# Optimization experiments

Hardware: AMD Instinct MI355X
Metric: run time of the kernel (lower is better)

Reference implementation:

```python
import jax, jax.numpy as jnp
import numpy as np

N = 50000
E = 800000
IN_CH = 128
HID = 64
HEADS = 4
OUT_CH = 64
NEG_SLOPE = 0.2


def add_self_loops(edge_index, num_nodes):
    loops = jnp.arange(num_nodes, dtype=edge_index.dtype)
    src = jnp.concatenate([edge_index[0], loops])
    dst = jnp.concatenate([edge_index[1], loops])
    return src, dst


def gat_layer(x, src, dst, W, a_src, a_dst, b, heads, out_ch, concat):
    n = x.shape[0]
    h = (x @ W).reshape(n, heads, out_ch)              # [N,H,C]
    al_src = jnp.einsum('nhc,hc->nh', h, a_src)        # [N,H]
    al_dst = jnp.einsum('nhc,hc->nh', h, a_dst)        # [N,H]
    e = jax.nn.leaky_relu(al_src[src] + al_dst[dst], NEG_SLOPE)  # [Et,H]
    # segment softmax over incoming edges of each destination node
    m = jax.ops.segment_max(e, dst, num_segments=n)
    ex = jnp.exp(e - m[dst])
    denom = jax.ops.segment_sum(ex, dst, num_segments=n)
    alpha = ex / (denom[dst] + 1e-16)                  # [Et,H]
    msg = h[src] * alpha[:, :, None]                   # [Et,H,C]
    out = jax.ops.segment_sum(msg, dst, num_segments=n)  # [N,H,C]
    if concat:
        out = out.reshape(n, heads * out_ch)
    else:
        out = out.mean(axis=1)
    return out + b


def setup_inputs() -> dict:
    key = jax.random.key(0)
    ks = jax.random.split(key, 10)
    x = jax.random.normal(ks[0], (N, IN_CH), dtype=jnp.float32)
    edge_index = jax.random.randint(ks[1], (2, E), 0, N, dtype=jnp.int64)
    s1 = 1.0 / np.sqrt(IN_CH)
    W1 = jax.random.normal(ks[2], (IN_CH, HEADS * HID), dtype=jnp.float32) * s1
    a_src1 = jax.random.normal(ks[3], (HEADS, HID), dtype=jnp.float32) * 0.1
    a_dst1 = jax.random.normal(ks[4], (HEADS, HID), dtype=jnp.float32) * 0.1
    b1 = jnp.zeros((HEADS * HID,), dtype=jnp.float32)
    s2 = 1.0 / np.sqrt(HEADS * HID)
    W2 = jax.random.normal(ks[5], (HEADS * HID, OUT_CH), dtype=jnp.float32) * s2
    a_src2 = jax.random.normal(ks[6], (1, OUT_CH), dtype=jnp.float32) * 0.1
    a_dst2 = jax.random.normal(ks[7], (1, OUT_CH), dtype=jnp.float32) * 0.1
    b2 = jnp.zeros((OUT_CH,), dtype=jnp.float32)
    return {"x": x, "edge_index": edge_index, "W1": W1, "a_src1": a_src1,
            "a_dst1": a_dst1, "b1": b1, "W2": W2, "a_src2": a_src2,
            "a_dst2": a_dst2, "b2": b2}


def reference(x, edge_index, W1, a_src1, a_dst1, b1, W2, a_src2, a_dst2, b2):
    src, dst = add_self_loops(edge_index, x.shape[0])
    h = gat_layer(x, src, dst, W1, a_src1, a_dst1, b1, HEADS, HID, True)
    h = jax.nn.elu(h)
    h = gat_layer(h, src, dst, W2, a_src2, a_dst2, b2, 1, OUT_CH, False)
    return jax.nn.elu(h)
```

## Files before the change

### kernel.cpp

```cpp
#include <hip/hip_runtime.h>
#include <hip/hip_bf16.h>
#include <cstdint>
#include <cstddef>


typedef float f32x4 __attribute__((ext_vector_type(4)));
typedef __fp16 f16x8 __attribute__((ext_vector_type(8)));
typedef __fp16 f16x4 __attribute__((ext_vector_type(4)));

static __device__ __forceinline__ float lrelu02(float x) { return x > 0.f ? x : 0.2f * x; }
static __device__ __forceinline__ float eluf(float x)    { return x > 0.f ? x : __expf(x) - 1.f; }

__global__ void detect_kernel(const int* __restrict__ ei, int* __restrict__ flag, int e) {
    int lane = threadIdx.x;
    int m = e < 64 ? e : 64;
    int z = (lane < m && ei[2 * lane + 1] == 0) ? 1 : 0;
    unsigned long long bal = __ballot(z);
    if (lane == 0) *flag = (__popcll(bal) >= m / 2 + 1) ? 1 : 0;
}

__global__ void hist_kernel(const int* __restrict__ ei, const int* __restrict__ flag,
                            int* __restrict__ deg, int e) {
    int i = blockIdx.x * 256 + threadIdx.x;
    if (i < e) {
        int f = *flag;
        int d = f ? ei[2 * (e + i)] : ei[e + i];
        atomicAdd(&deg[d], 1);
    }
}

__global__ __launch_bounds__(256) void scan_blocks_kernel(const int* __restrict__ deg,
                                                          int* __restrict__ loc,
                                                          int* __restrict__ bsum, int n) {
    __shared__ int wsum[4];
    int t = threadIdx.x, lane = t & 63, w = t >> 6;
    int base = blockIdx.x * 1024 + t * 4;
    int4 v = make_int4(0, 0, 0, 0);
    if (base + 3 < n) {
        v = *(const int4*)(deg + base);
        v.x += 1; v.y += 1; v.z += 1; v.w += 1;
    } else {
        if (base < n) v.x = deg[base] + 1;
        if (base + 1 < n) v.y = deg[base + 1] + 1;
        if (base + 2 < n) v.z = deg[base + 2] + 1;
        if (base + 3 < n) v.w = deg[base + 3] + 1;
    }
    int s = v.x + v.y + v.z + v.w;
    int incl = s;
    #pragma unroll
    for (int d = 1; d < 64; d <<= 1) { int o = __shfl_up(incl, d); if (lane >= d) incl += o; }
    if (lane == 63) wsum[w] = incl;
    __syncthreads();
    int woff = 0;
    for (int k = 0; k < w; ++k) woff += wsum[k];
    int excl = woff + incl - s;
    if (base < n) {
        int e0 = excl, e1 = e0 + v.x, e2 = e1 + v.y, e3 = e2 + v.z;
        loc[base] = e0;
        if (base + 1 < n) loc[base + 1] = e1;
        if (base + 2 < n) loc[base + 2] = e2;
        if (base + 3 < n) loc[base + 3] = e3;
    }
    if (t == 255) bsum[blockIdx.x] = woff + incl;
}

__global__ __launch_bounds__(256) void scan_sums_kernel(const int* __restrict__ bsum,
                                                        int* __restrict__ boff, int nb,
                                                        int* __restrict__ rowptr, int n) {
    __shared__ int ws[4];
    int t = threadIdx.x, lane = t & 63, w = t >> 6;
    int v = (t < nb) ? bsum[t] : 0;
    int incl = v;
    #pragma unroll
    for (int d = 1; d < 64; d <<= 1) { int o = __shfl_up(incl, d); if (lane >= d) incl += o; }
    if (lane == 63) ws[w] = incl;
    __syncthreads();
    int woff = 0;
    for (int k = 0; k < w; ++k) woff += ws[k];
    int excl = woff + incl - v;
    if (t < nb) boff[t] = excl;
    if (t == nb - 1) rowptr[n] = excl + v;
}

__global__ void scan_add_kernel(int* __restrict__ rowptr, const int* __restrict__ boff,
                                int* __restrict__ cursor, int n) {
    int i = blockIdx.x * 256 + threadIdx.x;
    if (i < n) {
        int v = rowptr[i] + boff[i >> 10];
        rowptr[i] = v;
        cursor[i] = v;
    }
}

__global__ void scatter_kernel(const int* __restrict__ ei, const int* __restrict__ flag,
                               int* __restrict__ cursor, int* __restrict__ sidx,
                               int e, int et) {
    int i = blockIdx.x * 256 + threadIdx.x;
    if (i >= et) return;
    int s, d;
    if (i < e) {
        int f = *flag;
        s = f ? ei[2 * i] : ei[i];
        d = f ? ei[2 * (e + i)] : ei[e + i];
    } else { s = d = i - e; }
    int pos = atomicAdd(&cursor[d], 1);
    sidx[pos] = s;
}

__global__ void prep_kernel(const float* __restrict__ W1, const float* __restrict__ W2,
                            __fp16* __restrict__ w1t, __fp16* __restrict__ w2t) {
    int i = blockIdx.x * 256 + threadIdx.x;
    if (i < 32768) {
        int nn = i >> 7, k = i & 127;
        w1t[i] = (__fp16)W1[k * 256 + nn];
    } else {
        int j = i - 32768;
        int nn = j >> 8, k = j & 255;
        w2t[j] = (__fp16)W2[k * 64 + nn];
    }
}

__global__ __launch_bounds__(256) void gemm1_kernel(const float* __restrict__ A,
                                                    const __fp16* __restrict__ w1t,
                                                    __fp16* __restrict__ C,
                                                    const float* __restrict__ a_src,
                                                    const float* __restrict__ a_dst,
                                                    float* __restrict__ als,
                                                    float* __restrict__ ald, int M) {
    __shared__ __fp16 sm[24064];
    #define AS(r, c)  sm[(r) * 72 + (c)]
    #define BST(r, c) sm[4608 + (r) * 72 + (c)]
    #define CS(r, c)  sm[(r) * 264 + (c)]
    float* sa = (float*)(sm + 23040);
    float* sd = (float*)(sm + 23552);
    int t = threadIdx.x;
    int wv = t >> 6, l = t & 63;
    int lm = l & 15, kq = l >> 4;
    int bm = blockIdx.x * 64;
    sa[t] = a_src[t];
    sd[t] = a_dst[t];
    f32x4 zero = {0.f, 0.f, 0.f, 0.f};
    f32x4 acc[4][4] = {{zero, zero, zero, zero}, {zero, zero, zero, zero},
                       {zero, zero, zero, zero}, {zero, zero, zero, zero}};
    int arow = t >> 2, akp = (t & 3) * 16;
    for (int k0 = 0; k0 < 128; k0 += 64) {
        {
            int gr = bm + arow;
            f16x8 av0, av1;
            if (gr < M) {
                const float* ap = A + (size_t)gr * 128 + k0 + akp;
                float4 a0 = *(const float4*)(ap + 0);
                float4 a1 = *(const float4*)(ap + 4);
                float4 a2 = *(const float4*)(ap + 8);
                float4 a3 = *(const float4*)(ap + 12);
                av0[0] = (__fp16)a0.x; av0[1] = (__fp16)a0.y; av0[2] = (__fp16)a0.z; av0[3] = (__fp16)a0.w;
                av0[4] = (__fp16)a1.x; av0[5] = (__fp16)a1.y; av0[6] = (__fp16)a1.z; av0[7] = (__fp16)a1.w;
                av1[0] = (__fp16)a2.x; av1[1] = (__fp16)a2.y; av1[2] = (__fp16)a2.z; av1[3] = (__fp16)a2.w;
                av1[4] = (__fp16)a3.x; av1[5] = (__fp16)a3.y; av1[6] = (__fp16)a3.z; av1[7] = (__fp16)a3.w;
            } else {
                f16x8 z = {0,0,0,0,0,0,0,0}; av0 = z; av1 = z;
            }
            *(f16x8*)&AS(arow, akp) = av0;
            *(f16x8*)&AS(arow, akp + 8) = av1;
        }
        {
            const __fp16* bp = w1t + (size_t)t * 128 + k0;
            #pragma unroll
            for (int c = 0; c < 8; ++c)
                *(f16x8*)&BST(t, c * 8) = *(const f16x8*)(bp + c * 8);
        }
        __syncthreads();
        #pragma unroll
        for (int ki = 0; ki < 2; ++ki) {
            int kc = ki * 32 + kq * 8;
            f16x8 af[4];
            #pragma unroll
            for (int mt = 0; mt < 4; ++mt) af[mt] = *(const f16x8*)&AS(mt * 16 + lm, kc);
            #pragma unroll
            for (int nt = 0; nt < 4; ++nt) {
                f16x8 bfrag = *(const f16x8*)&BST(wv * 64 + nt * 16 + lm, kc);
                #pragma unroll
                for (int mt = 0; mt < 4; ++mt)
                    acc[mt][nt] = __builtin_amdgcn_mfma_f32_16x16x32_f16(af[mt], bfrag, acc[mt][nt], 0, 0, 0);
            }
        }
        __syncthreads();
    }
    #pragma unroll
    for (int mt = 0; mt < 4; ++mt)
        #pragma unroll
        for (int nt = 0; nt < 4; ++nt)
            #pragma unroll
            for (int r = 0; r < 4; ++r)
                CS(mt * 16 + kq * 4 + r, wv * 64 + nt * 16 + lm) = (__fp16)acc[mt][nt][r];
    __syncthreads();
    {
        int row = t >> 2, head = t & 3;
        int gr = bm + row;
        f16x8 c[8];
        #pragma unroll
        for (int q = 0; q < 8; ++q) c[q] = *(const f16x8*)&CS(row, head * 64 + q * 8);
        float ps = 0.f, pd = 0.f;
        #pragma unroll
        for (int q = 0; q < 8; ++q)
            #pragma unroll
            for (int j = 0; j < 8; ++j) {
                float v = (float)c[q][j];
                ps += v * sa[head * 64 + q * 8 + j];
                pd += v * sd[head * 64 + q * 8 + j];
            }
        if (gr < M) {
            f16x8* gp = (f16x8*)(C + (size_t)gr * 256 + head * 64);
            #pragma unroll
            for (int q = 0; q < 8; ++q) gp[q] = c[q];
            als[gr * 4 + head] = ps;
            ald[gr * 4 + head] = pd;
        }
    }
    #undef AS
    #undef BST
    #undef CS
}

__global__ __launch_bounds__(256) void gemm2_kernel(const __fp16* __restrict__ A,
                                                    const __fp16* __restrict__ w2t,
                                                    __fp16* __restrict__ C,
                                                    const float* __restrict__ a_src,
                                                    const float* __restrict__ a_dst,
                                                    float* __restrict__ als,
                                                    float* __restrict__ ald, int M) {
    __shared__ __fp16 sm[9216];
    #define AS(r, c)  sm[(r) * 72 + (c)]
    #define BST(r, c) sm[4608 + (r) * 72 + (c)]
    #define CS(r, c)  sm[(r) * 72 + (c)]
    int t = threadIdx.x;
    int wv = t >> 6, l = t & 63;
    int lm = l & 15, kq = l >> 4;
    int bm = blockIdx.x * 64;
    f32x4 zero = {0.f, 0.f, 0.f, 0.f};
    f32x4 acc[4] = {zero, zero, zero, zero};
    int arow = t >> 2, akp = (t & 3) * 16;
    int bn = t & 63, bkc = (t >> 6) * 16;
    for (int k0 = 0; k0 < 256; k0 += 64) {
        {
            int gr = bm + arow;
            f16x8 av0, av1;
            if (gr < M) {
                const __fp16* ap = A + (size_t)gr * 256 + k0 + akp;
                av0 = *(const f16x8*)(ap);
                av1 = *(const f16x8*)(ap + 8);
            } else { f16x8 z = {0,0,0,0,0,0,0,0}; av0 = z; av1 = z; }
            *(f16x8*)&AS(arow, akp) = av0;
            *(f16x8*)&AS(arow, akp + 8) = av1;
        }
        {
            const __fp16* bp = w2t + (size_t)bn * 256 + k0 + bkc;
            *(f16x8*)&BST(bn, bkc) = *(const f16x8*)(bp);
            *(f16x8*)&BST(bn, bkc + 8) = *(const f16x8*)(bp + 8);
        }
        __syncthreads();
        #pragma unroll
        for (int ki = 0; ki < 2; ++ki) {
            int kc = ki * 32 + kq * 8;
            f16x8 bfrag = *(const f16x8*)&BST(wv * 16 + lm, kc);
            #pragma unroll
            for (int mt = 0; mt < 4; ++mt) {
                f16x8 afrag = *(const f16x8*)&AS(mt * 16 + lm, kc);
                acc[mt] = __builtin_amdgcn_mfma_f32_16x16x32_f16(afrag, bfrag, acc[mt], 0, 0, 0);
            }
        }
        __syncthreads();
    }
    #pragma unroll
    for (int mt = 0; mt < 4; ++mt)
        #pragma unroll
        for (int r = 0; r < 4; ++r)
            CS(mt * 16 + kq * 4 + r, wv * 16 + lm) = (__fp16)acc[mt][r];
    __syncthreads();
    {
        int row = t >> 2, ch = (t & 3) * 16;
        int gr = bm + row;
        f16x8 c0 = *(const f16x8*)&CS(row, ch);
        f16x8 c1 = *(const f16x8*)&CS(row, ch + 8);
        if (gr < M) {
            f16x8* gp = (f16x8*)(C + (size_t)gr * 64 + ch);
            gp[0] = c0; gp[1] = c1;
        }
        float ps = 0.f, pd = 0.f;
        #pragma unroll
        for (int j = 0; j < 8; ++j) {
            float v0 = (float)c0[j], v1 = (float)c1[j];
            ps += v0 * a_src[ch + j] + v1 * a_src[ch + 8 + j];
            pd += v0 * a_dst[ch + j] + v1 * a_dst[ch + 8 + j];
        }
        ps += __shfl_down(ps, 2); ps += __shfl_down(ps, 1);
        pd += __shfl_down(pd, 2); pd += __shfl_down(pd, 1);
        if ((t & 3) == 0 && gr < M) {
            als[gr] = ps;
            ald[gr] = pd;
        }
    }
    #undef AS
    #undef BST
    #undef CS
}

__global__ __launch_bounds__(256) void agg1_kernel(const __fp16* __restrict__ h1,
                                                   const int* __restrict__ sidx,
                                                   const int* __restrict__ rowptr,
                                                   const float* __restrict__ als,
                                                   const float* __restrict__ ald,
                                                   const float* __restrict__ b1,
                                                   __fp16* __restrict__ x2, int n) {
    int t = threadIdx.x, wv = t >> 6, l = t & 63;
    int node = blockIdx.x * 4 + wv;
    if (node >= n) return;
    int le = l & 31, halfE = l >> 5;
    int head = le >> 3;
    float aldn = ald[node * 4 + head];
    int p0 = rowptr[node], p1 = rowptr[node + 1];
    float acc[8] = {0.f, 0.f, 0.f, 0.f, 0.f, 0.f, 0.f, 0.f};
    float accw = 0.f;
    auto body = [&](int p) {
        int s = sidx[p];
        float wt = __expf(lrelu02(als[s * 4 + head] + aldn));
        accw += wt;
        f16x8 r = *(const f16x8*)(h1 + (size_t)s * 256 + le * 8);
        #pragma unroll
        for (int j = 0; j < 8; ++j) acc[j] += wt * (float)r[j];
    };
    int p = p0 + halfE;
    for (; p + 6 < p1; p += 8) { body(p); body(p + 2); body(p + 4); body(p + 6); }
    for (; p < p1; p += 2) body(p);
    #pragma unroll
    for (int j = 0; j < 8; ++j) acc[j] += __shfl_down(acc[j], 32);
    accw += __shfl_down(accw, 32);
    if (l < 32) {
        float rd = 1.f / (accw + 1e-16f);
        f16x8 o;
        #pragma unroll
        for (int j = 0; j < 8; ++j) {
            float v = acc[j] * rd + b1[le * 8 + j];
            o[j] = (__fp16)eluf(v);
        }
        *(f16x8*)(x2 + (size_t)node * 256 + le * 8) = o;
    }
}

__global__ __launch_bounds__(256) void agg2_kernel(const __fp16* __restrict__ h2,
                                                   const int* __restrict__ sidx,
                                                   const int* __restrict__ rowptr,
                                                   const float* __restrict__ als,
                                                   const float* __restrict__ ald,
                                                   const float* __restrict__ b2,
                                                   float* __restrict__ out, int n) {
    int t = threadIdx.x, wv = t >> 6, l = t & 63;
    int node = blockIdx.x * 4 + wv;
    if (node >= n) return;
    int slot = l >> 3, cq = l & 7;
    float aldn = ald[node];
    int p0 = rowptr[node], p1 = rowptr[node + 1];
    float acc[8] = {0.f, 0.f, 0.f, 0.f, 0.f, 0.f, 0.f, 0.f};
    float accw = 0.f;
    auto body = [&](int p) {
        int s = sidx[p];
        float wt = __expf(lrelu02(als[s] + aldn));
        accw += wt;
        f16x8 r = *(const f16x8*)(h2 + (size_t)s * 64 + cq * 8);
        #pragma unroll
        for (int j = 0; j < 8; ++j) acc[j] += wt * (float)r[j];
    };
    int p = p0 + slot;
    for (; p + 8 < p1; p += 16) { body(p); body(p + 8); }
    if (p < p1) body(p);
    #pragma unroll
    for (int j = 0; j < 8; ++j) {
        acc[j] += __shfl_down(acc[j], 32);
        acc[j] += __shfl_down(acc[j], 16);
        acc[j] += __shfl_down(acc[j], 8);
    }
    accw += __shfl_down(accw, 32);
    accw += __shfl_down(accw, 16);
    accw += __shfl_down(accw, 8);
    if (l < 8) {
        float rd = 1.f / (accw + 1e-16f);
        float4 o0, o1;
        o0.x = eluf(acc[0] * rd + b2[cq * 8 + 0]);
        o0.y = eluf(acc[1] * rd + b2[cq * 8 + 1]);
        o0.z = eluf(acc[2] * rd + b2[cq * 8 + 2]);
        o0.w = eluf(acc[3] * rd + b2[cq * 8 + 3]);
        o1.x = eluf(acc[4] * rd + b2[cq * 8 + 4]);
        o1.y = eluf(acc[5] * rd + b2[cq * 8 + 5]);
        o1.z = eluf(acc[6] * rd + b2[cq * 8 + 6]);
        o1.w = eluf(acc[7] * rd + b2[cq * 8 + 7]);
        float4* gp = (float4*)(out + (size_t)node * 64 + cq * 8);
        gp[0] = o0; gp[1] = o1;
    }
}

extern "C" void kernel_launch(void* const* d_in, const int* in_sizes, int n_in,
                              void* d_out, int out_size, void* d_ws, size_t ws_size,
                              hipStream_t stream) {
    const float* x   = (const float*)d_in[0];
    const int*   ei  = (const int*)d_in[1];
    const float* W1  = (const float*)d_in[2];
    const float* as1 = (const float*)d_in[3];
    const float* ad1 = (const float*)d_in[4];
    const float* b1  = (const float*)d_in[5];
    const float* W2  = (const float*)d_in[6];
    const float* as2 = (const float*)d_in[7];
    const float* ad2 = (const float*)d_in[8];
    const float* b2  = (const float*)d_in[9];
    float* out = (float*)d_out;

    const int n  = in_sizes[0] / 128;
    const int e  = in_sizes[1] / 2;
    const int et = e + n;

    char* w = (char*)d_ws;
    size_t off = 0;
    auto take = [&](size_t bytes) -> void* {
        void* p = w + off;
        off = (off + bytes + 255) & ~(size_t)255;
        return p;
    };
    __fp16* h1h = (__fp16*)take((size_t)n * 256 * 2);
    __fp16* x2h = (__fp16*)take((size_t)n * 256 * 2);
    __fp16* h2h = (__fp16*)take((size_t)n * 64 * 2);
    __fp16* w1t = (__fp16*)take((size_t)256 * 128 * 2);
    __fp16* w2t = (__fp16*)take((size_t)64 * 256 * 2);
    float* al1s = (float*)take((size_t)n * 4 * 4);
    float* al1d = (float*)take((size_t)n * 4 * 4);
    float* al2s = (float*)take((size_t)n * 4);
    float* al2d = (float*)take((size_t)n * 4);
    int* deg    = (int*)take((size_t)(n + 1) * 4);
    int* rowptr = (int*)take((size_t)(n + 1) * 4);
    int* cursor = (int*)take((size_t)(n + 1) * 4);
    int* sidx   = (int*)take((size_t)et * 4);
    int* bsum   = (int*)take(1024);
    int* boff   = (int*)take(1024);
    int* flag   = (int*)take(256);

    detect_kernel<<<1, 64, 0, stream>>>(ei, flag, e);
    hipMemsetAsync(deg, 0, (size_t)n * 4, stream);
    prep_kernel<<<192, 256, 0, stream>>>(W1, W2, w1t, w2t);
    hist_kernel<<<(e + 255) / 256, 256, 0, stream>>>(ei, flag, deg, e);
    int nb = (n + 1023) / 1024;
    scan_blocks_kernel<<<nb, 256, 0, stream>>>(deg, rowptr, bsum, n);
    scan_sums_kernel<<<1, 256, 0, stream>>>(bsum, boff, nb, rowptr, n);
    scan_add_kernel<<<(n + 255) / 256, 256, 0, stream>>>(rowptr, boff, cursor, n);
    scatter_kernel<<<(et + 255) / 256, 256, 0, stream>>>(ei, flag, cursor, sidx, e, et);

    const int mblocks = (n + 63) / 64;
    const int nodeblocks = (n + 3) / 4;

    gemm1_kernel<<<mblocks, 256, 0, stream>>>(x, w1t, h1h, as1, ad1, al1s, al1d, n);
    agg1_kernel<<<nodeblocks, 256, 0, stream>>>(h1h, sidx, rowptr, al1s, al1d, b1, x2h, n);

    gemm2_kernel<<<mblocks, 256, 0, stream>>>(x2h, w2t, h2h, as2, ad2, al2s, al2d, n);
    agg2_kernel<<<nodeblocks, 256, 0, stream>>>(h2h, sidx, rowptr, al2s, al2d, b2, out, n);
}
```

Measured before the change: 310.3 us.

## Fuse layer-1 aggregation with layer-2 GEMM and trim CSR-build launches

Layer-1 aggregation now writes each 32-node block's ELU output into shared memory, and the layer-2 projection runs there with MFMA. This removes the x2 intermediate's global write and read and one kernel launch. The edge-layout detect kernel, the deg memset and the block-sum scan kernel are folded into neighbouring kernels: each block recomputes the layout flag, and scan_add loops over the block sums. The agg2 loop is unrolled further. The fused kernel uses 512 threads with large shared memory, which may lower occupancy during the gather-heavy aggregation.

```diff
diff --git a/kernel.cpp b/kernel.cpp
--- a/kernel.cpp
+++ b/kernel.cpp
@@ -6,24 +6,45 @@
 
 typedef float f32x4 __attribute__((ext_vector_type(4)));
 typedef __fp16 f16x8 __attribute__((ext_vector_type(8)));
-typedef __fp16 f16x4 __attribute__((ext_vector_type(4)));
 
 static __device__ __forceinline__ float lrelu02(float x) { return x > 0.f ? x : 0.2f * x; }
 static __device__ __forceinline__ float eluf(float x)    { return x > 0.f ? x : __expf(x) - 1.f; }
 
-__global__ void detect_kernel(const int* __restrict__ ei, int* __restrict__ flag, int e) {
-    int lane = threadIdx.x;
-    int m = e < 64 ? e : 64;
-    int z = (lane < m && ei[2 * lane + 1] == 0) ? 1 : 0;
-    unsigned long long bal = __ballot(z);
-    if (lane == 0) *flag = (__popcll(bal) >= m / 2 + 1) ? 1 : 0;
-}
-
-__global__ void hist_kernel(const int* __restrict__ ei, const int* __restrict__ flag,
-                            int* __restrict__ deg, int e) {
+static __device__ __forceinline__ int block_flag(const int* __restrict__ ei, int e,
+                                                 int* sflag) {
+    int t = threadIdx.x;
+    if (t < 64) {
+        int m = e < 64 ? e : 64;
+        int z = (t < m && ei[2 * t + 1] == 0) ? 1 : 0;
+        unsigned long long bal = __ballot(z);
+        if (t == 0) *sflag = (__popcll(bal) >= m / 2 + 1) ? 1 : 0;
+    }
+    __syncthreads();
+    return *sflag;
+}
+
+__global__ void prep_kernel(const float* __restrict__ W1, const float* __restrict__ W2,
+                            __fp16* __restrict__ w1t, __fp16* __restrict__ w2t,
+                            int* __restrict__ deg, int n) {
+    int i = blockIdx.x * 256 + threadIdx.x;
+    if (i < 32768) {
+        int nn = i >> 7, k = i & 127;
+        w1t[i] = (__fp16)W1[k * 256 + nn];
+    } else if (i < 49152) {
+        int j = i - 32768;
+        int nn = j >> 8, k = j & 255;
+        w2t[j] = (__fp16)W2[k * 64 + nn];
+    } else if (i - 49152 <= n) {
+        deg[i - 49152] = 0;
+    }
+}
+
+__global__ __launch_bounds__(256) void hist_kernel(const int* __restrict__ ei,
+                                                   int* __restrict__ deg, int e) {
+    __shared__ int sflag;
+    int f = block_flag(ei, e, &sflag);
     int i = blockIdx.x * 256 + threadIdx.x;
     if (i < e) {
-        int f = *flag;
         int d = f ? ei[2 * (e + i)] : ei[e + i];
         atomicAdd(&deg[d], 1);
     }
@@ -64,60 +85,38 @@
     if (t == 255) bsum[blockIdx.x] = woff + incl;
 }
 
-__global__ __launch_bounds__(256) void scan_sums_kernel(const int* __restrict__ bsum,
-                                                        int* __restrict__ boff, int nb,
-                                                        int* __restrict__ rowptr, int n) {
-    __shared__ int ws[4];
-    int t = threadIdx.x, lane = t & 63, w = t >> 6;
-    int v = (t < nb) ? bsum[t] : 0;
-    int incl = v;
-    #pragma unroll
-    for (int d = 1; d < 64; d <<= 1) { int o = __shfl_up(incl, d); if (lane >= d) incl += o; }
-    if (lane == 63) ws[w] = incl;
-    __syncthreads();
-    int woff = 0;
-    for (int k = 0; k < w; ++k) woff += ws[k];
-    int excl = woff + incl - v;
-    if (t < nb) boff[t] = excl;
-    if (t == nb - 1) rowptr[n] = excl + v;
-}
-
-__global__ void scan_add_kernel(int* __restrict__ rowptr, const int* __restrict__ boff,
-                                int* __restrict__ cursor, int n) {
+__global__ void scan_add_kernel(int* __restrict__ rowptr, const int* __restrict__ bsum,
+                                int* __restrict__ cursor, int n, int nb) {
     int i = blockIdx.x * 256 + threadIdx.x;
     if (i < n) {
-        int v = rowptr[i] + boff[i >> 10];
+        int chunk = i >> 10;
+        int off = 0;
+        for (int k = 0; k < chunk; ++k) off += bsum[k];
+        int v = rowptr[i] + off;
         rowptr[i] = v;
         cursor[i] = v;
-    }
-}
-
-__global__ void scatter_kernel(const int* __restrict__ ei, const int* __restrict__ flag,
-                               int* __restrict__ cursor, int* __restrict__ sidx,
-                               int e, int et) {
+    } else if (i == n) {
+        int tot = 0;
+        for (int k = 0; k < nb; ++k) tot += bsum[k];
+        rowptr[n] = tot;
+    }
+}
+
+__global__ __launch_bounds__(256) void scatter_kernel(const int* __restrict__ ei,
+                                                      int* __restrict__ cursor,
+                                                      int* __restrict__ sidx,
+                                                      int e, int et) {
+    __shared__ int sflag;
+    int f = block_flag(ei, e, &sflag);
     int i = blockIdx.x * 256 + threadIdx.x;
     if (i >= et) return;
     int s, d;
     if (i < e) {
-        int f = *flag;
         s = f ? ei[2 * i] : ei[i];
         d = f ? ei[2 * (e + i)] : ei[e + i];
     } else { s = d = i - e; }
     int pos = atomicAdd(&cursor[d], 1);
     sidx[pos] = s;
-}
-
-__global__ void prep_kernel(const float* __restrict__ W1, const float* __restrict__ W2,
-                            __fp16* __restrict__ w1t, __fp16* __restrict__ w2t) {
-    int i = blockIdx.x * 256 + threadIdx.x;
-    if (i < 32768) {
-        int nn = i >> 7, k = i & 127;
-        w1t[i] = (__fp16)W1[k * 256 + nn];
-    } else {
-        int j = i - 32768;
-        int nn = j >> 8, k = j & 255;
-        w2t[j] = (__fp16)W2[k * 64 + nn];
-    }
 }
 
 __global__ __launch_bounds__(256) void gemm1_kernel(const float* __restrict__ A,
@@ -222,129 +221,106 @@
     #undef CS
 }
 
-__global__ __launch_bounds__(256) void gemm2_kernel(const __fp16* __restrict__ A,
-                                                    const __fp16* __restrict__ w2t,
-                                                    __fp16* __restrict__ C,
-                                                    const float* __restrict__ a_src,
-                                                    const float* __restrict__ a_dst,
-                                                    float* __restrict__ als,
-                                                    float* __restrict__ ald, int M) {
-    __shared__ __fp16 sm[9216];
-    #define AS(r, c)  sm[(r) * 72 + (c)]
-    #define BST(r, c) sm[4608 + (r) * 72 + (c)]
-    #define CS(r, c)  sm[(r) * 72 + (c)]
-    int t = threadIdx.x;
-    int wv = t >> 6, l = t & 63;
+__global__ __launch_bounds__(512) void agg1g2_kernel(const __fp16* __restrict__ h1,
+                                                     const int* __restrict__ sidx,
+                                                     const int* __restrict__ rowptr,
+                                                     const float* __restrict__ als,
+                                                     const float* __restrict__ ald,
+                                                     const float* __restrict__ b1,
+                                                     const __fp16* __restrict__ w2t,
+                                                     const float* __restrict__ a_src2,
+                                                     const float* __restrict__ a_dst2,
+                                                     __fp16* __restrict__ h2,
+                                                     float* __restrict__ al2s,
+                                                     float* __restrict__ al2d, int n) {
+    __shared__ __fp16 X[32 * 264];
+    __shared__ __fp16 Bs[64 * 264];
+    #define XS(r, c)  X[(r) * 264 + (c)]
+    #define BS2(r, c) Bs[(r) * 264 + (c)]
+    #define CS2(r, c) X[(r) * 72 + (c)]
+    int t = threadIdx.x, wv = t >> 6, l = t & 63;
+    int bm = blockIdx.x * 32;
+    {
+        int nn = t >> 3, kc = (t & 7) * 32;
+        const __fp16* bp = w2t + (size_t)nn * 256 + kc;
+        #pragma unroll
+        for (int c = 0; c < 4; ++c)
+            *(f16x8*)&BS2(nn, kc + c * 8) = *(const f16x8*)(bp + c * 8);
+    }
+    int le = l & 31, halfE = l >> 5, head = le >> 3;
+    #pragma unroll
+    for (int q = 0; q < 4; ++q) {
+        int row = wv * 4 + q;
+        int node = bm + row;
+        float acc[8] = {0.f, 0.f, 0.f, 0.f, 0.f, 0.f, 0.f, 0.f};
+        float accw = 0.f;
+        if (node < n) {
+            float aldn = ald[node * 4 + head];
+            int p0 = rowptr[node], p1 = rowptr[node + 1];
+            auto body = [&](int p) {
+                int s = sidx[p];
+                float wt = __expf(lrelu02(als[s * 4 + head] + aldn));
+                accw += wt;
+                f16x8 r = *(const f16x8*)(h1 + (size_t)s * 256 + le * 8);
+                #pragma unroll
+                for (int j = 0; j < 8; ++j) acc[j] += wt * (float)r[j];
+            };
+            int p = p0 + halfE;
+            for (; p + 6 < p1; p += 8) { body(p); body(p + 2); body(p + 4); body(p + 6); }
+            for (; p < p1; p += 2) body(p);
+        }
+        #pragma unroll
+        for (int j = 0; j < 8; ++j) acc[j] += __shfl_down(acc[j], 32);
+        accw += __shfl_down(accw, 32);
+        if (l < 32) {
+            f16x8 o;
+            if (node < n) {
+                float rd = 1.f / (accw + 1e-16f);
+                #pragma unroll
+                for (int j = 0; j < 8; ++j)
+                    o[j] = (__fp16)eluf(acc[j] * rd + b1[le * 8 + j]);
+            } else {
+                f16x8 z = {0,0,0,0,0,0,0,0}; o = z;
+            }
+            *(f16x8*)&XS(row, le * 8) = o;
+        }
+    }
+    __syncthreads();
     int lm = l & 15, kq = l >> 4;
-    int bm = blockIdx.x * 64;
-    f32x4 zero = {0.f, 0.f, 0.f, 0.f};
-    f32x4 acc[4] = {zero, zero, zero, zero};
-    int arow = t >> 2, akp = (t & 3) * 16;
-    int bn = t & 63, bkc = (t >> 6) * 16;
-    for (int k0 = 0; k0 < 256; k0 += 64) {
-        {
-            int gr = bm + arow;
-            f16x8 av0, av1;
-            if (gr < M) {
-                const __fp16* ap = A + (size_t)gr * 256 + k0 + akp;
-                av0 = *(const f16x8*)(ap);
-                av1 = *(const f16x8*)(ap + 8);
-            } else { f16x8 z = {0,0,0,0,0,0,0,0}; av0 = z; av1 = z; }
-            *(f16x8*)&AS(arow, akp) = av0;
-            *(f16x8*)&AS(arow, akp + 8) = av1;
-        }
-        {
-            const __fp16* bp = w2t + (size_t)bn * 256 + k0 + bkc;
-            *(f16x8*)&BST(bn, bkc) = *(const f16x8*)(bp);
-            *(f16x8*)&BST(bn, bkc + 8) = *(const f16x8*)(bp + 8);
-        }
-        __syncthreads();
-        #pragma unroll
-        for (int ki = 0; ki < 2; ++ki) {
-            int kc = ki * 32 + kq * 8;
-            f16x8 bfrag = *(const f16x8*)&BST(wv * 16 + lm, kc);
-            #pragma unroll
-            for (int mt = 0; mt < 4; ++mt) {
-                f16x8 afrag = *(const f16x8*)&AS(mt * 16 + lm, kc);
-                acc[mt] = __builtin_amdgcn_mfma_f32_16x16x32_f16(afrag, bfrag, acc[mt], 0, 0, 0);
-            }
-        }
-        __syncthreads();
-    }
-    #pragma unroll
-    for (int mt = 0; mt < 4; ++mt)
-        #pragma unroll
-        for (int r = 0; r < 4; ++r)
-            CS(mt * 16 + kq * 4 + r, wv * 16 + lm) = (__fp16)acc[mt][r];
-    __syncthreads();
-    {
-        int row = t >> 2, ch = (t & 3) * 16;
+    int mt = wv >> 2, nt = wv & 3;
+    f32x4 acc2 = {0.f, 0.f, 0.f, 0.f};
+    #pragma unroll
+    for (int kc = 0; kc < 8; ++kc) {
+        f16x8 af = *(const f16x8*)&XS(mt * 16 + lm, kc * 32 + kq * 8);
+        f16x8 bf = *(const f16x8*)&BS2(nt * 16 + lm, kc * 32 + kq * 8);
+        acc2 = __builtin_amdgcn_mfma_f32_16x16x32_f16(af, bf, acc2, 0, 0, 0);
+    }
+    __syncthreads();
+    #pragma unroll
+    for (int r = 0; r < 4; ++r)
+        CS2(mt * 16 + kq * 4 + r, nt * 16 + lm) = (__fp16)acc2[r];
+    __syncthreads();
+    if (t < 256) {
+        int row = t >> 3, ch = (t & 7) * 8;
         int gr = bm + row;
-        f16x8 c0 = *(const f16x8*)&CS(row, ch);
-        f16x8 c1 = *(const f16x8*)&CS(row, ch + 8);
-        if (gr < M) {
-            f16x8* gp = (f16x8*)(C + (size_t)gr * 64 + ch);
-            gp[0] = c0; gp[1] = c1;
-        }
+        f16x8 c0 = *(const f16x8*)&CS2(row, ch);
         float ps = 0.f, pd = 0.f;
         #pragma unroll
         for (int j = 0; j < 8; ++j) {
-            float v0 = (float)c0[j], v1 = (float)c1[j];
-            ps += v0 * a_src[ch + j] + v1 * a_src[ch + 8 + j];
-            pd += v0 * a_dst[ch + j] + v1 * a_dst[ch + 8 + j];
-        }
-        ps += __shfl_down(ps, 2); ps += __shfl_down(ps, 1);
-        pd += __shfl_down(pd, 2); pd += __shfl_down(pd, 1);
-        if ((t & 3) == 0 && gr < M) {
-            als[gr] = ps;
-            ald[gr] = pd;
-        }
-    }
-    #undef AS
-    #undef BST
-    #undef CS
-}
-
-__global__ __launch_bounds__(256) void agg1_kernel(const __fp16* __restrict__ h1,
-                                                   const int* __restrict__ sidx,
-                                                   const int* __restrict__ rowptr,
-                                                   const float* __restrict__ als,
-                                                   const float* __restrict__ ald,
-                                                   const float* __restrict__ b1,
-                                                   __fp16* __restrict__ x2, int n) {
-    int t = threadIdx.x, wv = t >> 6, l = t & 63;
-    int node = blockIdx.x * 4 + wv;
-    if (node >= n) return;
-    int le = l & 31, halfE = l >> 5;
-    int head = le >> 3;
-    float aldn = ald[node * 4 + head];
-    int p0 = rowptr[node], p1 = rowptr[node + 1];
-    float acc[8] = {0.f, 0.f, 0.f, 0.f, 0.f, 0.f, 0.f, 0.f};
-    float accw = 0.f;
-    auto body = [&](int p) {
-        int s = sidx[p];
-        float wt = __expf(lrelu02(als[s * 4 + head] + aldn));
-        accw += wt;
-        f16x8 r = *(const f16x8*)(h1 + (size_t)s * 256 + le * 8);
-        #pragma unroll
-        for (int j = 0; j < 8; ++j) acc[j] += wt * (float)r[j];
-    };
-    int p = p0 + halfE;
-    for (; p + 6 < p1; p += 8) { body(p); body(p + 2); body(p + 4); body(p + 6); }
-    for (; p < p1; p += 2) body(p);
-    #pragma unroll
-    for (int j = 0; j < 8; ++j) acc[j] += __shfl_down(acc[j], 32);
-    accw += __shfl_down(accw, 32);
-    if (l < 32) {
-        float rd = 1.f / (accw + 1e-16f);
-        f16x8 o;
-        #pragma unroll
-        for (int j = 0; j < 8; ++j) {
-            float v = acc[j] * rd + b1[le * 8 + j];
-            o[j] = (__fp16)eluf(v);
-        }
-        *(f16x8*)(x2 + (size_t)node * 256 + le * 8) = o;
-    }
+            float v = (float)c0[j];
+            ps += v * a_src2[ch + j];
+            pd += v * a_dst2[ch + j];
+        }
+        ps += __shfl_down(ps, 4); ps += __shfl_down(ps, 2); ps += __shfl_down(ps, 1);
+        pd += __shfl_down(pd, 4); pd += __shfl_down(pd, 2); pd += __shfl_down(pd, 1);
+        if (gr < n) {
+            *(f16x8*)(h2 + (size_t)gr * 64 + ch) = c0;
+            if ((t & 7) == 0) { al2s[gr] = ps; al2d[gr] = pd; }
+        }
+    }
+    #undef XS
+    #undef BS2
+    #undef CS2
 }
 
 __global__ __launch_bounds__(256) void agg2_kernel(const __fp16* __restrict__ h2,
@@ -371,8 +347,8 @@
         for (int j = 0; j < 8; ++j) acc[j] += wt * (float)r[j];
     };
     int p = p0 + slot;
-    for (; p + 8 < p1; p += 16) { body(p); body(p + 8); }
-    if (p < p1) body(p);
+    for (; p + 24 < p1; p += 32) { body(p); body(p + 8); body(p + 16); body(p + 24); }
+    for (; p < p1; p += 8) body(p);
     #pragma unroll
     for (int j = 0; j < 8; ++j) {
         acc[j] += __shfl_down(acc[j], 32);
@@ -425,7 +401,6 @@
         return p;
     };
     __fp16* h1h = (__fp16*)take((size_t)n * 256 * 2);
-    __fp16* x2h = (__fp16*)take((size_t)n * 256 * 2);
     __fp16* h2h = (__fp16*)take((size_t)n * 64 * 2);
     __fp16* w1t = (__fp16*)take((size_t)256 * 128 * 2);
     __fp16* w2t = (__fp16*)take((size_t)64 * 256 * 2);
@@ -438,25 +413,17 @@
     int* cursor = (int*)take((size_t)(n + 1) * 4);
     int* sidx   = (int*)take((size_t)et * 4);
     int* bsum   = (int*)take(1024);
-    int* boff   = (int*)take(1024);
-    int* flag   = (int*)take(256);
-
-    detect_kernel<<<1, 64, 0, stream>>>(ei, flag, e);
-    hipMemsetAsync(deg, 0, (size_t)n * 4, stream);
-    prep_kernel<<<192, 256, 0, stream>>>(W1, W2, w1t, w2t);
-    hist_kernel<<<(e + 255) / 256, 256, 0, stream>>>(ei, flag, deg, e);
+
     int nb = (n + 1023) / 1024;
+
+    prep_kernel<<<(49152 + n + 1 + 255) / 256, 256, 0, stream>>>(W1, W2, w1t, w2t, deg, n);
+    hist_kernel<<<(e + 255) / 256, 256, 0, stream>>>(ei, deg, e);
     scan_blocks_kernel<<<nb, 256, 0, stream>>>(deg, rowptr, bsum, n);
-    scan_sums_kernel<<<1, 256, 0, stream>>>(bsum, boff, nb, rowptr, n);
-    scan_add_kernel<<<(n + 255) / 256, 256, 0, stream>>>(rowptr, boff, cursor, n);
-    scatter_kernel<<<(et + 255) / 256, 256, 0, stream>>>(ei, flag, cursor, sidx, e, et);
-
-    const int mblocks = (n + 63) / 64;
-    const int nodeblocks = (n + 3) / 4;
-
-    gemm1_kernel<<<mblocks, 256, 0, stream>>>(x, w1t, h1h, as1, ad1, al1s, al1d, n);
-    agg1_kernel<<<nodeblocks, 256, 0, stream>>>(h1h, sidx, rowptr, al1s, al1d, b1, x2h, n);
-
-    gemm2_kernel<<<mblocks, 256, 0, stream>>>(x2h, w2t, h2h, as2, ad2, al2s, al2d, n);
-    agg2_kernel<<<nodeblocks, 256, 0, stream>>>(h2h, sidx, rowptr, al2s, al2d, b2, out, n);
-}
+    scan_add_kernel<<<(n + 1 + 255) / 256, 256, 0, stream>>>(rowptr, bsum, cursor, n, nb);
+    scatter_kernel<<<(et + 255) / 256, 256, 0, stream>>>(ei, cursor, sidx, e, et);
+
+    gemm1_kernel<<<(n + 63) / 64, 256, 0, stream>>>(x, w1t, h1h, as1, ad1, al1s, al1d, n);
+    agg1g2_kernel<<<(n + 31) / 32, 512, 0, stream>>>(h1h, sidx, rowptr, al1s, al1d, b1,
+                                                     w2t, as2, ad2, h2h, al2s, al2d, n);
+    agg2_kernel<<<(n + 3) / 4, 256, 0, stream>>>(h2h, sidx, rowptr, al2s, al2d, b2, out, n);
+}
```

New measurement: 314.6 us. About the same (+1.4%).

## Fuse GEMM1, histogram and weight prep into one launch; drop scan and detect kernels

Applied to the files above, without the earlier changes.

Merges the first-layer GEMM, the degree histogram and the W2 transpose into a single heterogeneous launch, with W1 converted to fp16 on the fly inside the GEMM. The separate detect, prep and scan_sums kernels go away: each block computes the layout flag itself, and scan_add sums the block partials serially. The aim is to cut launch count and serial dependencies between small kernels. The GEMM K-tile shrinks to 32, W1 is now read with strided fp32 loads in every block, and agg2 is unrolled deeper.

```diff
diff --git a/kernel.cpp b/kernel.cpp
--- a/kernel.cpp
+++ b/kernel.cpp
@@ -6,27 +6,138 @@
 
 typedef float f32x4 __attribute__((ext_vector_type(4)));
 typedef __fp16 f16x8 __attribute__((ext_vector_type(8)));
-typedef __fp16 f16x4 __attribute__((ext_vector_type(4)));
 
 static __device__ __forceinline__ float lrelu02(float x) { return x > 0.f ? x : 0.2f * x; }
 static __device__ __forceinline__ float eluf(float x)    { return x > 0.f ? x : __expf(x) - 1.f; }
 
-__global__ void detect_kernel(const int* __restrict__ ei, int* __restrict__ flag, int e) {
-    int lane = threadIdx.x;
-    int m = e < 64 ? e : 64;
-    int z = (lane < m && ei[2 * lane + 1] == 0) ? 1 : 0;
-    unsigned long long bal = __ballot(z);
-    if (lane == 0) *flag = (__popcll(bal) >= m / 2 + 1) ? 1 : 0;
-}
-
-__global__ void hist_kernel(const int* __restrict__ ei, const int* __restrict__ flag,
-                            int* __restrict__ deg, int e) {
-    int i = blockIdx.x * 256 + threadIdx.x;
-    if (i < e) {
-        int f = *flag;
-        int d = f ? ei[2 * (e + i)] : ei[e + i];
-        atomicAdd(&deg[d], 1);
-    }
+static __device__ __forceinline__ int block_flag(const int* __restrict__ ei, int e,
+                                                 int* sflag) {
+    int t = threadIdx.x;
+    if (t < 64) {
+        int m = e < 64 ? e : 64;
+        int z = (t < m && ei[2 * t + 1] == 0) ? 1 : 0;
+        unsigned long long bal = __ballot(z);
+        if (t == 0) *sflag = (__popcll(bal) >= m / 2 + 1) ? 1 : 0;
+    }
+    __syncthreads();
+    return *sflag;
+}
+
+__global__ __launch_bounds__(256) void k1_kernel(const float* __restrict__ A,
+                                                 const float* __restrict__ W1,
+                                                 __fp16* __restrict__ C,
+                                                 const float* __restrict__ a_src,
+                                                 const float* __restrict__ a_dst,
+                                                 float* __restrict__ als,
+                                                 float* __restrict__ ald,
+                                                 const int* __restrict__ ei,
+                                                 int* __restrict__ deg,
+                                                 const float* __restrict__ W2,
+                                                 __fp16* __restrict__ w2t,
+                                                 int M, int e, int gb, int hb) {
+    __shared__ __fp16 sm[17920];
+    int b = blockIdx.x;
+    int t = threadIdx.x;
+    if (b >= gb) {
+        if (b < gb + hb) {
+            int f = block_flag(ei, e, (int*)sm);
+            int i = (b - gb) * 256 + t;
+            if (i < e) {
+                int d = f ? ei[2 * (e + i)] : ei[e + i];
+                atomicAdd(&deg[d], 1);
+            }
+        } else {
+            int j = (b - gb - hb) * 256 + t;
+            if (j < 16384) {
+                int nn = j >> 8, k = j & 255;
+                w2t[j] = (__fp16)W2[k * 64 + nn];
+            }
+        }
+        return;
+    }
+    #define AS(r, c)  sm[(r) * 40 + (c)]
+    #define BST(r, c) sm[2560 + (r) * 40 + (c)]
+    #define CS(r, c)  sm[(r) * 264 + (c)]
+    float* sa = (float*)(sm + 16896);
+    float* sd = (float*)(sm + 17408);
+    int wv = t >> 6, l = t & 63;
+    int lm = l & 15, kq = l >> 4;
+    int bm = b * 64;
+    sa[t] = a_src[t];
+    sd[t] = a_dst[t];
+    f32x4 zero = {0.f, 0.f, 0.f, 0.f};
+    f32x4 acc[4][4] = {{zero, zero, zero, zero}, {zero, zero, zero, zero},
+                       {zero, zero, zero, zero}, {zero, zero, zero, zero}};
+    int arow = t >> 2, achunk = (t & 3) * 8;
+    for (int k0 = 0; k0 < 128; k0 += 32) {
+        {
+            int gr = bm + arow;
+            f16x8 av;
+            if (gr < M) {
+                const float* ap = A + (size_t)gr * 128 + k0 + achunk;
+                float4 a0 = *(const float4*)(ap + 0);
+                float4 a1 = *(const float4*)(ap + 4);
+                av[0] = (__fp16)a0.x; av[1] = (__fp16)a0.y; av[2] = (__fp16)a0.z; av[3] = (__fp16)a0.w;
+                av[4] = (__fp16)a1.x; av[5] = (__fp16)a1.y; av[6] = (__fp16)a1.z; av[7] = (__fp16)a1.w;
+            } else { f16x8 z = {0,0,0,0,0,0,0,0}; av = z; }
+            *(f16x8*)&AS(arow, achunk) = av;
+        }
+        {
+            #pragma unroll
+            for (int bc = 0; bc < 4; ++bc) {
+                f16x8 bh;
+                #pragma unroll
+                for (int j = 0; j < 8; ++j)
+                    bh[j] = (__fp16)W1[(size_t)(k0 + bc * 8 + j) * 256 + t];
+                *(f16x8*)&BST(t, bc * 8) = bh;
+            }
+        }
+        __syncthreads();
+        #pragma unroll
+        for (int nt = 0; nt < 4; ++nt) {
+            f16x8 bfrag = *(const f16x8*)&BST(wv * 64 + nt * 16 + lm, kq * 8);
+            #pragma unroll
+            for (int mt = 0; mt < 4; ++mt) {
+                f16x8 afrag = *(const f16x8*)&AS(mt * 16 + lm, kq * 8);
+                acc[mt][nt] = __builtin_amdgcn_mfma_f32_16x16x32_f16(afrag, bfrag, acc[mt][nt], 0, 0, 0);
+            }
+        }
+        __syncthreads();
+    }
+    #pragma unroll
+    for (int mt = 0; mt < 4; ++mt)
+        #pragma unroll
+        for (int nt = 0; nt < 4; ++nt)
+            #pragma unroll
+            for (int r = 0; r < 4; ++r)
+                CS(mt * 16 + kq * 4 + r, wv * 64 + nt * 16 + lm) = (__fp16)acc[mt][nt][r];
+    __syncthreads();
+    {
+        int row = t >> 2, head = t & 3;
+        int gr = bm + row;
+        f16x8 c[8];
+        #pragma unroll
+        for (int q = 0; q < 8; ++q) c[q] = *(const f16x8*)&CS(row, head * 64 + q * 8);
+        float ps = 0.f, pd = 0.f;
+        #pragma unroll
+        for (int q = 0; q < 8; ++q)
+            #pragma unroll
+            for (int j = 0; j < 8; ++j) {
+                float v = (float)c[q][j];
+                ps += v * sa[head * 64 + q * 8 + j];
+                pd += v * sd[head * 64 + q * 8 + j];
+            }
+        if (gr < M) {
+            f16x8* gp = (f16x8*)(C + (size_t)gr * 256 + head * 64);
+            #pragma unroll
+            for (int q = 0; q < 8; ++q) gp[q] = c[q];
+            als[gr * 4 + head] = ps;
+            ald[gr * 4 + head] = pd;
+        }
+    }
+    #undef AS
+    #undef BST
+    #undef CS
 }
 
 __global__ __launch_bounds__(256) void scan_blocks_kernel(const int* __restrict__ deg,
@@ -64,42 +175,33 @@
     if (t == 255) bsum[blockIdx.x] = woff + incl;
 }
 
-__global__ __launch_bounds__(256) void scan_sums_kernel(const int* __restrict__ bsum,
-                                                        int* __restrict__ boff, int nb,
-                                                        int* __restrict__ rowptr, int n) {
-    __shared__ int ws[4];
-    int t = threadIdx.x, lane = t & 63, w = t >> 6;
-    int v = (t < nb) ? bsum[t] : 0;
-    int incl = v;
-    #pragma unroll
-    for (int d = 1; d < 64; d <<= 1) { int o = __shfl_up(incl, d); if (lane >= d) incl += o; }
-    if (lane == 63) ws[w] = incl;
-    __syncthreads();
-    int woff = 0;
-    for (int k = 0; k < w; ++k) woff += ws[k];
-    int excl = woff + incl - v;
-    if (t < nb) boff[t] = excl;
-    if (t == nb - 1) rowptr[n] = excl + v;
-}
-
-__global__ void scan_add_kernel(int* __restrict__ rowptr, const int* __restrict__ boff,
-                                int* __restrict__ cursor, int n) {
+__global__ void scan_add_kernel(int* __restrict__ rowptr, const int* __restrict__ bsum,
+                                int* __restrict__ cursor, int n, int nb) {
     int i = blockIdx.x * 256 + threadIdx.x;
     if (i < n) {
-        int v = rowptr[i] + boff[i >> 10];
+        int chunk = i >> 10;
+        int off = 0;
+        for (int k = 0; k < chunk; ++k) off += bsum[k];
+        int v = rowptr[i] + off;
         rowptr[i] = v;
         cursor[i] = v;
-    }
-}
-
-__global__ void scatter_kernel(const int* __restrict__ ei, const int* __restrict__ flag,
-                               int* __restrict__ cursor, int* __restrict__ sidx,
-                               int e, int et) {
+    } else if (i == n) {
+        int tot = 0;
+        for (int k = 0; k < nb; ++k) tot += bsum[k];
+        rowptr[n] = tot;
+    }
+}
+
+__global__ __launch_bounds__(256) void scatter_kernel(const int* __restrict__ ei,
+                                                      int* __restrict__ cursor,
+                                                      int* __restrict__ sidx,
+                                                      int e, int et) {
+    __shared__ int sflag;
+    int f = block_flag(ei, e, &sflag);
     int i = blockIdx.x * 256 + threadIdx.x;
     if (i >= et) return;
     int s, d;
     if (i < e) {
-        int f = *flag;
         s = f ? ei[2 * i] : ei[i];
         d = f ? ei[2 * (e + i)] : ei[e + i];
     } else { s = d = i - e; }
@@ -107,119 +209,46 @@
     sidx[pos] = s;
 }
 
-__global__ void prep_kernel(const float* __restrict__ W1, const float* __restrict__ W2,
-                            __fp16* __restrict__ w1t, __fp16* __restrict__ w2t) {
-    int i = blockIdx.x * 256 + threadIdx.x;
-    if (i < 32768) {
-        int nn = i >> 7, k = i & 127;
-        w1t[i] = (__fp16)W1[k * 256 + nn];
-    } else {
-        int j = i - 32768;
-        int nn = j >> 8, k = j & 255;
-        w2t[j] = (__fp16)W2[k * 64 + nn];
-    }
-}
-
-__global__ __launch_bounds__(256) void gemm1_kernel(const float* __restrict__ A,
-                                                    const __fp16* __restrict__ w1t,
-                                                    __fp16* __restrict__ C,
-                                                    const float* __restrict__ a_src,
-                                                    const float* __restrict__ a_dst,
-                                                    float* __restrict__ als,
-                                                    float* __restrict__ ald, int M) {
-    __shared__ __fp16 sm[24064];
-    #define AS(r, c)  sm[(r) * 72 + (c)]
-    #define BST(r, c) sm[4608 + (r) * 72 + (c)]
-    #define CS(r, c)  sm[(r) * 264 + (c)]
-    float* sa = (float*)(sm + 23040);
-    float* sd = (float*)(sm + 23552);
-    int t = threadIdx.x;
-    int wv = t >> 6, l = t & 63;
-    int lm = l & 15, kq = l >> 4;
-    int bm = blockIdx.x * 64;
-    sa[t] = a_src[t];
-    sd[t] = a_dst[t];
-    f32x4 zero = {0.f, 0.f, 0.f, 0.f};
-    f32x4 acc[4][4] = {{zero, zero, zero, zero}, {zero, zero, zero, zero},
-                       {zero, zero, zero, zero}, {zero, zero, zero, zero}};
-    int arow = t >> 2, akp = (t & 3) * 16;
-    for (int k0 = 0; k0 < 128; k0 += 64) {
-        {
-            int gr = bm + arow;
-            f16x8 av0, av1;
-            if (gr < M) {
-                const float* ap = A + (size_t)gr * 128 + k0 + akp;
-                float4 a0 = *(const float4*)(ap + 0);
-                float4 a1 = *(const float4*)(ap + 4);
-                float4 a2 = *(const float4*)(ap + 8);
-                float4 a3 = *(const float4*)(ap + 12);
-                av0[0] = (__fp16)a0.x; av0[1] = (__fp16)a0.y; av0[2] = (__fp16)a0.z; av0[3] = (__fp16)a0.w;
-                av0[4] = (__fp16)a1.x; av0[5] = (__fp16)a1.y; av0[6] = (__fp16)a1.z; av0[7] = (__fp16)a1.w;
-                av1[0] = (__fp16)a2.x; av1[1] = (__fp16)a2.y; av1[2] = (__fp16)a2.z; av1[3] = (__fp16)a2.w;
-                av1[4] = (__fp16)a3.x; av1[5] = (__fp16)a3.y; av1[6] = (__fp16)a3.z; av1[7] = (__fp16)a3.w;
-            } else {
-                f16x8 z = {0,0,0,0,0,0,0,0}; av0 = z; av1 = z;
-            }
-            *(f16x8*)&AS(arow, akp) = av0;
-            *(f16x8*)&AS(arow, akp + 8) = av1;
-        }
-        {
-            const __fp16* bp = w1t + (size_t)t * 128 + k0;
-            #pragma unroll
-            for (int c = 0; c < 8; ++c)
-                *(f16x8*)&BST(t, c * 8) = *(const f16x8*)(bp + c * 8);
-        }
-        __syncthreads();
-        #pragma unroll
-        for (int ki = 0; ki < 2; ++ki) {
-            int kc = ki * 32 + kq * 8;
-            f16x8 af[4];
-            #pragma unroll
-            for (int mt = 0; mt < 4; ++mt) af[mt] = *(const f16x8*)&AS(mt * 16 + lm, kc);
-            #pragma unroll
-            for (int nt = 0; nt < 4; ++nt) {
-                f16x8 bfrag = *(const f16x8*)&BST(wv * 64 + nt * 16 + lm, kc);
-                #pragma unroll
-                for (int mt = 0; mt < 4; ++mt)
-                    acc[mt][nt] = __builtin_amdgcn_mfma_f32_16x16x32_f16(af[mt], bfrag, acc[mt][nt], 0, 0, 0);
-            }
-        }
-        __syncthreads();
-    }
+__global__ __launch_bounds__(256) void agg1_kernel(const __fp16* __restrict__ h1,
+                                                   const int* __restrict__ sidx,
+                                                   const int* __restrict__ rowptr,
+                                                   const float* __restrict__ als,
+                                                   const float* __restrict__ ald,
+                                                   const float* __restrict__ b1,
+                                                   __fp16* __restrict__ x2, int n) {
+    int t = threadIdx.x, wv = t >> 6, l = t & 63;
+    int node = blockIdx.x * 4 + wv;
+    if (node >= n) return;
+    int le = l & 31, halfE = l >> 5;
+    int head = le >> 3;
+    float aldn = ald[node * 4 + head];
+    int p0 = rowptr[node], p1 = rowptr[node + 1];
+    float acc[8] = {0.f, 0.f, 0.f, 0.f, 0.f, 0.f, 0.f, 0.f};
+    float accw = 0.f;
+    auto body = [&](int p) {
+        int s = sidx[p];
+        float wt = __expf(lrelu02(als[s * 4 + head] + aldn));
+        accw += wt;
+        f16x8 r = *(const f16x8*)(h1 + (size_t)s * 256 + le * 8);
+        #pragma unroll
+        for (int j = 0; j < 8; ++j) acc[j] += wt * (float)r[j];
+    };
+    int p = p0 + halfE;
+    for (; p + 6 < p1; p += 8) { body(p); body(p + 2); body(p + 4); body(p + 6); }
+    for (; p < p1; p += 2) body(p);
     #pragma unroll
-    for (int mt = 0; mt < 4; ++mt)
-        #pragma unroll
-        for (int nt = 0; nt < 4; ++nt)
-            #pragma unroll
-            for (int r = 0; r < 4; ++r)
-                CS(mt * 16 + kq * 4 + r, wv * 64 + nt * 16 + lm) = (__fp16)acc[mt][nt][r];
-    __syncthreads();
-    {
-        int row = t >> 2, head = t & 3;
-        int gr = bm + row;
-        f16x8 c[8];
-        #pragma unroll
-        for (int q = 0; q < 8; ++q) c[q] = *(const f16x8*)&CS(row, head * 64 + q * 8);
-        float ps = 0.f, pd = 0.f;
-        #pragma unroll
-        for (int q = 0; q < 8; ++q)
-            #pragma unroll
-            for (int j = 0; j < 8; ++j) {
-                float v = (float)c[q][j];
-                ps += v * sa[head * 64 + q * 8 + j];
-                pd += v * sd[head * 64 + q * 8 + j];
-            }
-        if (gr < M) {
-            f16x8* gp = (f16x8*)(C + (size_t)gr * 256 + head * 64);
-            #pragma unroll
-            for (int q = 0; q < 8; ++q) gp[q] = c[q];
-            als[gr * 4 + head] = ps;
-            ald[gr * 4 + head] = pd;
-        }
-    }
-    #undef AS
-    #undef BST
-    #undef CS
+    for (int j = 0; j < 8; ++j) acc[j] += __shfl_down(acc[j], 32);
+    accw += __shfl_down(accw, 32);
+    if (l < 32) {
+        float rd = 1.f / (accw + 1e-16f);
+        f16x8 o;
+        #pragma unroll
+        for (int j = 0; j < 8; ++j) {
+            float v = acc[j] * rd + b1[le * 8 + j];
+            o[j] = (__fp16)eluf(v);
+        }
+        *(f16x8*)(x2 + (size_t)node * 256 + le * 8) = o;
+    }
 }
 
 __global__ __launch_bounds__(256) void gemm2_kernel(const __fp16* __restrict__ A,
@@ -305,48 +334,6 @@
     #undef CS
 }
 
-__global__ __launch_bounds__(256) void agg1_kernel(const __fp16* __restrict__ h1,
-                                                   const int* __restrict__ sidx,
-                                                   const int* __restrict__ rowptr,
-                                                   const float* __restrict__ als,
-                                                   const float* __restrict__ ald,
-                                                   const float* __restrict__ b1,
-                                                   __fp16* __restrict__ x2, int n) {
-    int t = threadIdx.x, wv = t >> 6, l = t & 63;
-    int node = blockIdx.x * 4 + wv;
-    if (node >= n) return;
-    int le = l & 31, halfE = l >> 5;
-    int head = le >> 3;
-    float aldn = ald[node * 4 + head];
-    int p0 = rowptr[node], p1 = rowptr[node + 1];
-    float acc[8] = {0.f, 0.f, 0.f, 0.f, 0.f, 0.f, 0.f, 0.f};
-    float accw = 0.f;
-    auto body = [&](int p) {
-        int s = sidx[p];
-        float wt = __expf(lrelu02(als[s * 4 + head] + aldn));
-        accw += wt;
-        f16x8 r = *(const f16x8*)(h1 + (size_t)s * 256 + le * 8);
-        #pragma unroll
-        for (int j = 0; j < 8; ++j) acc[j] += wt * (float)r[j];
-    };
-    int p = p0 + halfE;
-    for (; p + 6 < p1; p += 8) { body(p); body(p + 2); body(p + 4); body(p + 6); }
-    for (; p < p1; p += 2) body(p);
-    #pragma unroll
-    for (int j = 0; j < 8; ++j) acc[j] += __shfl_down(acc[j], 32);
-    accw += __shfl_down(accw, 32);
-    if (l < 32) {
-        float rd = 1.f / (accw + 1e-16f);
-        f16x8 o;
-        #pragma unroll
-        for (int j = 0; j < 8; ++j) {
-            float v = acc[j] * rd + b1[le * 8 + j];
-            o[j] = (__fp16)eluf(v);
-        }
-        *(f16x8*)(x2 + (size_t)node * 256 + le * 8) = o;
-    }
-}
-
 __global__ __launch_bounds__(256) void agg2_kernel(const __fp16* __restrict__ h2,
                                                    const int* __restrict__ sidx,
                                                    const int* __restrict__ rowptr,
@@ -371,8 +358,8 @@
         for (int j = 0; j < 8; ++j) acc[j] += wt * (float)r[j];
     };
     int p = p0 + slot;
-    for (; p + 8 < p1; p += 16) { body(p); body(p + 8); }
-    if (p < p1) body(p);
+    for (; p + 24 < p1; p += 32) { body(p); body(p + 8); body(p + 16); body(p + 24); }
+    for (; p < p1; p += 8) body(p);
     #pragma unroll
     for (int j = 0; j < 8; ++j) {
         acc[j] += __shfl_down(acc[j], 32);
@@ -427,7 +414,6 @@
     __fp16* h1h = (__fp16*)take((size_t)n * 256 * 2);
     __fp16* x2h = (__fp16*)take((size_t)n * 256 * 2);
     __fp16* h2h = (__fp16*)take((size_t)n * 64 * 2);
-    __fp16* w1t = (__fp16*)take((size_t)256 * 128 * 2);
     __fp16* w2t = (__fp16*)take((size_t)64 * 256 * 2);
     float* al1s = (float*)take((size_t)n * 4 * 4);
     float* al1d = (float*)take((size_t)n * 4 * 4);
@@ -437,26 +423,20 @@
     int* rowptr = (int*)take((size_t)(n + 1) * 4);
     int* cursor = (int*)take((size_t)(n + 1) * 4);
     int* sidx   = (int*)take((size_t)et * 4);
-    int* bsum   = (int*)take(1024);
-    int* boff   = (int*)take(1024);
-    int* flag   = (int*)take(256);
-
-    detect_kernel<<<1, 64, 0, stream>>>(ei, flag, e);
-    hipMemsetAsync(deg, 0, (size_t)n * 4, stream);
-    prep_kernel<<<192, 256, 0, stream>>>(W1, W2, w1t, w2t);
-    hist_kernel<<<(e + 255) / 256, 256, 0, stream>>>(ei, flag, deg, e);
-    int nb = (n + 1023) / 1024;
+    int* bsum   = (int*)take(256);
+
+    const int gb = (n + 63) / 64;
+    const int hb = (e + 255) / 256;
+    const int pb = (16384 + 255) / 256;
+    const int nb = (n + 1023) / 1024;
+
+    hipMemsetAsync(deg, 0, (size_t)(n + 1) * 4, stream);
+    k1_kernel<<<gb + hb + pb, 256, 0, stream>>>(x, W1, h1h, as1, ad1, al1s, al1d,
+                                                ei, deg, W2, w2t, n, e, gb, hb);
     scan_blocks_kernel<<<nb, 256, 0, stream>>>(deg, rowptr, bsum, n);
-    scan_sums_kernel<<<1, 256, 0, stream>>>(bsum, boff, nb, rowptr, n);
-    scan_add_kernel<<<(n + 255) / 256, 256, 0, stream>>>(rowptr, boff, cursor, n);
-    scatter_kernel<<<(et + 255) / 256, 256, 0, stream>>>(ei, flag, cursor, sidx, e, et);
-
-    const int mblocks = (n + 63) / 64;
-    const int nodeblocks = (n + 3) / 4;
-
-    gemm1_kernel<<<mblocks, 256, 0, stream>>>(x, w1t, h1h, as1, ad1, al1s, al1d, n);
-    agg1_kernel<<<nodeblocks, 256, 0, stream>>>(h1h, sidx, rowptr, al1s, al1d, b1, x2h, n);
-
-    gemm2_kernel<<<mblocks, 256, 0, stream>>>(x2h, w2t, h2h, as2, ad2, al2s, al2d, n);
-    agg2_kernel<<<nodeblocks, 256, 0, stream>>>(h2h, sidx, rowptr, al2s, al2d, b2, out, n);
-}
+    scan_add_kernel<<<(n + 1 + 255) / 256, 256, 0, stream>>>(rowptr, bsum, cursor, n, nb);
+    scatter_kernel<<<(et + 255) / 256, 256, 0, stream>>>(ei, cursor, sidx, e, et);
+    agg1_kernel<<<(n + 3) / 4, 256, 0, stream>>>(h1h, sidx, rowptr, al1s, al1d, b1, x2h, n);
+    gemm2_kernel<<<(n + 63) / 64, 256, 0, stream>>>(x2h, w2t, h2h, as2, ad2, al2s, al2d, n);
+    agg2_kernel<<<(n + 3) / 4, 256, 0, stream>>>(h2h, sidx, rowptr, al2s, al2d, b2, out, n);
+}
```

New measurement: 290.3 us. 1.07x faster.
